# Optimization experiments

Measured on AMD Instinct MI355X. Metric: run time of the kernel, lower is better.

The kernel has to match this reference:

```python
import jax, jax.numpy as jnp
import numpy as np

D_MODEL = 1024
N_HEADS = 16
HEAD_DIM = D_MODEL // N_HEADS


def setup_inputs() -> dict:
    key = jax.random.key(0)
    k_x, k_qkv, k_out = jax.random.split(key, 3)
    B, T = 4, 2048
    x = jax.random.normal(k_x, (B, T, D_MODEL), dtype=jnp.float32)
    # nn.Linear weight is (out, in); we store transposed (in, out) for x @ W
    s = 1.0 / np.sqrt(D_MODEL)
    W_qkv = jax.random.uniform(k_qkv, (D_MODEL, 3 * D_MODEL), dtype=jnp.float32, minval=-s, maxval=s)
    W_out = jax.random.uniform(k_out, (D_MODEL, D_MODEL), dtype=jnp.float32, minval=-s, maxval=s)
    return {"x": x, "W_qkv": W_qkv, "W_out": W_out}


def reference(x, W_qkv, W_out):
    B, T, C = x.shape
    H, Dh = N_HEADS, HEAD_DIM
    qkv = x @ W_qkv                                   # (B,T,3C)
    q, k, v = jnp.split(qkv, 3, axis=-1)
    # (B,T,C) -> (B,H,T,Dh)
    def split_heads(t):
        return t.reshape(B, T, H, Dh).transpose(0, 2, 1, 3)
    q, k, v = split_heads(q), split_heads(k), split_heads(v)
    scale = 1.0 / np.sqrt(Dh).astype(np.float32)
    scores = jnp.einsum('bhqd,bhkd->bhqk', q, k) * scale  # (B,H,T,T)
    causal = jnp.triu(jnp.ones((T, T), dtype=bool), k=1)   # True above diag
    scores = jnp.where(causal, -jnp.inf, scores)
    attn = jax.nn.softmax(scores, axis=-1)
    out = jnp.einsum('bhqk,bhkd->bhqd', attn, v)       # (B,H,T,Dh)
    out = out.transpose(0, 2, 1, 3).reshape(B, T, C)
    return out @ W_out
```

## Files before the change

### kernel.cpp

```cpp
#include <hip/hip_runtime.h>
#include <stdint.h>

#define T_ 2048
#define BB_ 4

typedef __bf16 bf16x8 __attribute__((ext_vector_type(8)));
typedef float f32x4 __attribute__((ext_vector_type(4)));
typedef unsigned short u16x8 __attribute__((ext_vector_type(8)));
typedef unsigned int u32x2 __attribute__((ext_vector_type(2)));
typedef unsigned int u32x4 __attribute__((ext_vector_type(4)));

__device__ __forceinline__ unsigned short f2b(float f) {
    unsigned int u = __builtin_bit_cast(unsigned int, f);
    return (unsigned short)((u + 0x7fffu + ((u >> 16) & 1u)) >> 16);
}

__device__ __forceinline__ unsigned cvt_pk(float lo, float hi) {
    unsigned r;
    asm("v_cvt_pk_bf16_f32 %0, %1, %2" : "=v"(r) : "v"(lo), "v"(hi));
    return r;
}

__device__ __forceinline__ void gload16(const void* g, const void* lds) {
    __builtin_amdgcn_global_load_lds(
        (__attribute__((address_space(1))) void*)(uintptr_t)g,
        (__attribute__((address_space(3))) void*)(uintptr_t)(unsigned int)(uintptr_t)lds,
        16, 0, 0);
}

__device__ __forceinline__ bf16x8 ld_b8(const unsigned short* p) {
    return *(const bf16x8*)p;
}

#define MFMA16(a, b, c) __builtin_amdgcn_mfma_f32_16x16x32_bf16((a), (b), (c), 0, 0, 0)

__global__ __launch_bounds__(256) void k_cvt(const float* __restrict__ in,
                                             unsigned short* __restrict__ out, int n) {
    int i = (blockIdx.x * 256 + threadIdx.x) * 4;
    const int stride = gridDim.x * 256 * 4;
    for (; i < n; i += stride) {
        const float4 v = *(const float4*)(in + i);
        ushort4 o = make_ushort4(f2b(v.x), f2b(v.y), f2b(v.z), f2b(v.w));
        *(ushort4*)(out + i) = o;
    }
}

template <int K, int N>
__global__ __launch_bounds__(256) void k_cvt_T(const float* __restrict__ W,
                                               unsigned short* __restrict__ WT) {
    __shared__ unsigned short t_[64][72];
    const int nt = blockIdx.x % (N / 64), kt = blockIdx.x / (N / 64);
    const int tid = threadIdx.x;
    const int r = tid >> 2, c = (tid & 3) * 16;
    const float* src = W + (size_t)(kt * 64 + r) * N + nt * 64 + c;
#pragma unroll
    for (int j = 0; j < 16; j += 4) {
        float4 v = *(const float4*)(src + j);
        t_[r][c + j + 0] = f2b(v.x);
        t_[r][c + j + 1] = f2b(v.y);
        t_[r][c + j + 2] = f2b(v.z);
        t_[r][c + j + 3] = f2b(v.w);
    }
    __syncthreads();
    unsigned short* dst = WT + (size_t)(nt * 64 + r) * K + kt * 64 + c;
#pragma unroll
    for (int j = 0; j < 16; ++j) dst[j] = t_[c + j][r];
}

template <int MODE, int NCOLS>
__global__ __launch_bounds__(512, 2) void k_gemm256(
    const unsigned short* __restrict__ A, const unsigned short* __restrict__ Bt,
    void* __restrict__ Cv, unsigned short* __restrict__ vt2) {
    constexpr int K = 1024, NT = K / 64;
    __shared__ unsigned short Abuf[2][2][8192];
    __shared__ unsigned short Bbuf[2][8192];
    const int tid = threadIdx.x;
    const int lane = tid & 63, wid = tid >> 6;
    const int wr = wid >> 1, wc = wid & 1;
    const int l4 = lane >> 4, l15 = lane & 15;
    const int m0 = blockIdx.y * 256, n0 = blockIdx.x * 128;

    const int se0 = tid * 8, se1 = tid * 8 + 4096;
    const int r0_ = se0 >> 6, c0_ = (se0 & 63) ^ ((r0_ & 7) << 3);
    const int r1_ = se1 >> 6, c1_ = (se1 & 63) ^ ((r1_ & 7) << 3);

    f32x4 acc[4][4] = {};

    auto STAGE = [&](int t, int d) {
#pragma unroll
        for (int h = 0; h < 2; ++h) {
            const unsigned short* as = A + (size_t)(m0 + h * 128) * K + t * 64;
            gload16(as + (size_t)r0_ * K + c0_, &Abuf[d][h][se0]);
            gload16(as + (size_t)r1_ * K + c1_, &Abuf[d][h][se1]);
        }
        const unsigned short* bs = Bt + (size_t)n0 * K + t * 64;
        gload16(bs + (size_t)r0_ * K + c0_, &Bbuf[d][se0]);
        gload16(bs + (size_t)r1_ * K + c1_, &Bbuf[d][se1]);
    };

    auto swz = [](const unsigned short* base, int row, int col) {
        int byte = row * 128 + col * 2;
        byte ^= (row & 7) << 4;
        return (const unsigned short*)((const char*)base + byte);
    };

    STAGE(0, 0);
    STAGE(1, 1);
    for (int t = 0; t < NT; ++t) {
        if (t == NT - 1)
            asm volatile("s_waitcnt vmcnt(0)" ::: "memory");
        else
            asm volatile("s_waitcnt vmcnt(6)" ::: "memory");
        __builtin_amdgcn_sched_barrier(0);
        __builtin_amdgcn_s_barrier();
        __builtin_amdgcn_sched_barrier(0);
        const unsigned short* Ah = &Abuf[t & 1][wr >> 1][0];
        const unsigned short* Bh = &Bbuf[t & 1][0];
#pragma unroll
        for (int ks = 0; ks < 2; ++ks) {
            bf16x8 af[4], bfr[4];
#pragma unroll
            for (int m = 0; m < 4; ++m)
                af[m] = ld_b8(swz(Ah, (wr & 1) * 64 + m * 16 + l15, ks * 32 + l4 * 8));
#pragma unroll
            for (int n = 0; n < 4; ++n)
                bfr[n] = ld_b8(swz(Bh, wc * 64 + n * 16 + l15, ks * 32 + l4 * 8));
            __builtin_amdgcn_s_setprio(1);
#pragma unroll
            for (int m = 0; m < 4; ++m)
#pragma unroll
                for (int n = 0; n < 4; ++n)
                    acc[m][n] = MFMA16(af[m], bfr[n], acc[m][n]);
            __builtin_amdgcn_s_setprio(0);
            __builtin_amdgcn_sched_barrier(0);
        }
        __builtin_amdgcn_s_barrier();
        __builtin_amdgcn_sched_barrier(0);
        if (t + 2 < NT) STAGE(t + 2, t & 1);
    }

    const int crow0 = m0 + wr * 64 + l4 * 4;
    const int ccol0 = n0 + wc * 64 + l15;
    if (MODE == 0 && n0 >= 2048) {
#pragma unroll
        for (int m = 0; m < 4; ++m)
#pragma unroll
            for (int n = 0; n < 4; ++n) {
                const int row = crow0 + m * 16;
                const int c = ccol0 + n * 16 - 2048;
                const int b = row >> 11, tt = row & 2047;
                const int h = c >> 6, dh = c & 63;
                ushort4 o;
                o.x = f2b(acc[m][n][0]);
                o.y = f2b(acc[m][n][1]);
                o.z = f2b(acc[m][n][2]);
                o.w = f2b(acc[m][n][3]);
                *(ushort4*)(vt2 + (size_t)(b * 16 + h) * 131072 + (tt >> 2) * 256 +
                            dh * 4) = o;
            }
    } else {
#pragma unroll
        for (int m = 0; m < 4; ++m)
#pragma unroll
            for (int n = 0; n < 4; ++n)
#pragma unroll
                for (int r = 0; r < 4; ++r) {
                    const size_t idx =
                        (size_t)(crow0 + m * 16 + r) * NCOLS + ccol0 + n * 16;
                    if (MODE == 1)
                        ((float*)Cv)[idx] = acc[m][n][r];
                    else
                        ((unsigned short*)Cv)[idx] = f2b(acc[m][n][r]);
                }
    }
}

__global__ __launch_bounds__(256) void k_attn(const unsigned short* __restrict__ qkv,
                                              const unsigned short* __restrict__ vt2,
                                              unsigned short* __restrict__ ao) {
    __shared__ unsigned short Ks[2 * 4096];
    __shared__ unsigned short Vs[2 * 4096];
    const int bh = blockIdx.x & 63;
    const int p = blockIdx.x >> 6;
    const int b = bh >> 4, h = bh & 15;
    const int tid = threadIdx.x, lane = tid & 63, w = tid >> 6;
    const int l4 = lane >> 4, l15 = lane & 15;

    const int sr0 = w * 16 + (lane >> 3);
    const int scol = 8 * ((lane & 7) ^ (lane >> 3));
    const unsigned short* Kg = qkv + (size_t)(b * T_) * 3072 + 1024 + h * 64;

    const unsigned short* Vg = vt2 + (size_t)bh * 131072;
    const int s0v = (w * 2 + 0) * 2 + (lane >> 5);
    const int s1v = (w * 2 + 1) * 2 + (lane >> 5);
    const unsigned short* vsrc0 =
        Vg + (4 * (s0v & 3) + (s0v >> 2)) * 256 + (lane & 31) * 8;
    const unsigned short* vsrc1 =
        Vg + (4 * (s1v & 3) + (s1v >> 2)) * 256 + (lane & 31) * 8;

    for (int half = 0; half < 2; ++half) {
        const int qt = half ? p : 31 - p;

        const unsigned short* qb =
            qkv + (size_t)(b * T_ + qt * 64 + w * 16 + l15) * 3072 + h * 64;
        bf16x8 qf0, qf1;
        {
            const bf16x8 r0 = ld_b8(qb + l4 * 8);
            const bf16x8 r1 = ld_b8(qb + 32 + l4 * 8);
#pragma unroll
            for (int j = 0; j < 8; ++j) {
                qf0[j] = (__bf16)((float)r0[j] * 0.18033688f);
                qf1[j] = (__bf16)((float)r1[j] * 0.18033688f);
            }
        }

        float m_s = -1e30f, l_s = 0.f;
        f32x4 o[4] = {};

        auto STAGE = [&](int kt, int bi) {
            unsigned short* Kb = Ks + bi * 4096;
            unsigned short* Vb = Vs + bi * 4096;
            gload16(Kg + (size_t)(kt * 64 + sr0) * 3072 + scol, Kb + (w * 2) * 512);
            gload16(Kg + (size_t)(kt * 64 + sr0 + 8) * 3072 + scol, Kb + (w * 2 + 1) * 512);
            gload16(vsrc0 + kt * 4096, Vb + (w * 2) * 512);
            gload16(vsrc1 + kt * 4096, Vb + (w * 2 + 1) * 512);
        };

        auto COMPUTE = [&](int bi, bool masked) {
            const unsigned short* Kb = Ks + bi * 4096;
            const unsigned short* Vb = Vs + bi * 4096;
            float tv[4][4];
            __builtin_amdgcn_s_setprio(1);
#pragma unroll
            for (int i = 0; i < 4; ++i) {
                const int key = i * 16 + l15;
                const int sw = (key & 7) << 4;
                const bf16x8 kf0 = ld_b8(Kb + (key * 128 + ((l4 * 16) ^ sw)) / 2);
                const bf16x8 kf1 = ld_b8(Kb + (key * 128 + ((l4 * 16 + 64) ^ sw)) / 2);
                f32x4 sacc = {};
                sacc = MFMA16(kf0, qf0, sacc);
                sacc = MFMA16(kf1, qf1, sacc);
#pragma unroll
                for (int r = 0; r < 4; ++r) tv[i][r] = sacc[r];
            }
            __builtin_amdgcn_s_setprio(0);
            if (masked) {
#pragma unroll
                for (int i = 0; i < 4; ++i)
#pragma unroll
                    for (int r = 0; r < 4; ++r)
                        if (i * 16 + l4 * 4 + r > w * 16 + l15) tv[i][r] = -1e30f;
            }
            float mi[4];
#pragma unroll
            for (int i = 0; i < 4; ++i)
                mi[i] = fmaxf(fmaxf(tv[i][0], tv[i][1]), fmaxf(tv[i][2], tv[i][3]));
            float mx = fmaxf(fmaxf(mi[0], mi[1]), fmaxf(mi[2], mi[3]));
            mx = fmaxf(mx, __shfl_xor(mx, 16));
            mx = fmaxf(mx, __shfl_xor(mx, 32));
            if (__any(mx > m_s + 8.0f)) {
                const float mnew = fmaxf(m_s, mx);
                const float fac = __builtin_amdgcn_exp2f(m_s - mnew);
                m_s = mnew;
                l_s *= fac;
#pragma unroll
                for (int r = 0; r < 4; ++r) {
                    const float fr = __shfl(fac, (l4 << 4) | (l4 * 4 + r));
#pragma unroll
                    for (int ni = 0; ni < 4; ++ni) o[ni][r] *= fr;
                }
            }
            float rs = 0.f;
            unsigned pw[8];
#pragma unroll
            for (int i = 0; i < 4; ++i) {
                float pv[4];
#pragma unroll
                for (int r = 0; r < 4; ++r) {
                    pv[r] = __builtin_amdgcn_exp2f(tv[i][r] - m_s);
                    rs += pv[r];
                }
                pw[i * 2 + 0] = cvt_pk(pv[0], pv[1]);
                pw[i * 2 + 1] = cvt_pk(pv[2], pv[3]);
            }
            rs += __shfl_xor(rs, 16);
            rs += __shfl_xor(rs, 32);
            l_s += rs;
            __builtin_amdgcn_s_setprio(1);
#pragma unroll
            for (int st = 0; st < 2; ++st) {
                const u32x4 pk = {pw[st * 4 + 0], pw[st * 4 + 1], pw[st * 4 + 2],
                                  pw[st * 4 + 3]};
                const bf16x8 pf = __builtin_bit_cast(bf16x8, pk);
#pragma unroll
                for (int ni = 0; ni < 4; ++ni) {
                    const unsigned short* vb =
                        Vb + (l4 * 4 + st * 2) * 256 + (ni * 16 + l15) * 4;
                    const u32x2 va = *(const u32x2*)vb;
                    const u32x2 vc = *(const u32x2*)(vb + 256);
                    const u32x4 vv = {va.x, va.y, vc.x, vc.y};
                    const bf16x8 vf = __builtin_bit_cast(bf16x8, vv);
                    o[ni] = MFMA16(pf, vf, o[ni]);
                }
            }
            __builtin_amdgcn_s_setprio(0);
        };

        __syncthreads();
        STAGE(0, 0);
        __syncthreads();
        for (int kt = 0; kt < qt; ++kt) {
            STAGE(kt + 1, (kt + 1) & 1);
            COMPUTE(kt & 1, false);
            __syncthreads();
        }
        COMPUTE(qt & 1, true);

        unsigned short* aop = ao + (size_t)(b * T_ + qt * 64 + w * 16) * 1024 + h * 64;
#pragma unroll
        for (int r = 0; r < 4; ++r) {
            const float lr = __shfl(l_s, (l4 << 4) | (l4 * 4 + r));
            const float inv = 1.0f / lr;
#pragma unroll
            for (int ni = 0; ni < 4; ++ni)
                aop[(size_t)(l4 * 4 + r) * 1024 + ni * 16 + l15] = f2b(o[ni][r] * inv);
        }
    }
}

extern "C" void kernel_launch(void* const* d_in, const int* in_sizes, int n_in,
                              void* d_out, int out_size, void* d_ws, size_t ws_size,
                              hipStream_t stream) {
    (void)in_sizes; (void)n_in; (void)out_size; (void)ws_size;
    const float* x = (const float*)d_in[0];
    const float* Wqkv = (const float*)d_in[1];
    const float* Wout = (const float*)d_in[2];
    char* ws = (char*)d_ws;
    unsigned short* xb = (unsigned short*)(ws + 0);
    unsigned short* wqkvT = (unsigned short*)(ws + 16777216);
    unsigned short* woutT = (unsigned short*)(ws + 23068672);
    unsigned short* qkvb = (unsigned short*)(ws + 25165824);
    unsigned short* vt2 = (unsigned short*)(ws + 75497472);
    unsigned short* ao = (unsigned short*)(ws + 92274688);

    k_cvt<<<2048, 256, 0, stream>>>(x, xb, 4 * T_ * 1024);
    k_cvt_T<1024, 3072><<<16 * 48, 256, 0, stream>>>(Wqkv, wqkvT);
    k_cvt_T<1024, 1024><<<16 * 16, 256, 0, stream>>>(Wout, woutT);
    k_gemm256<0, 3072><<<dim3(24, 32), 512, 0, stream>>>(xb, wqkvT, qkvb, vt2);
    k_attn<<<1024, 256, 0, stream>>>(qkvb, vt2, ao);
    k_gemm256<1, 1024><<<dim3(8, 32), 512, 0, stream>>>(ao, woutT, d_out, nullptr);
}
```

Baseline: 168.3 us.

## Process two 64-row query tiles per attention block to reuse K/V tiles

Each attention block now handles a 128-row query tile (two 64-row sub-tiles per wave) instead of 64 rows, so every K/V tile staged into LDS feeds twice as many MFMAs. Causal masking is generalized to the two sub-tiles across the final two key tiles, and the grid is halved to 512 blocks while keeping the front/back pairing for load balance. The intent is to cut global-to-LDS traffic and per-tile sync overhead. In exchange, register pressure roughly doubles for accumulators and scores, and fewer blocks means lower parallelism on a large-CU device.

```diff
diff --git a/kernel.cpp b/kernel.cpp
--- a/kernel.cpp
+++ b/kernel.cpp
@@ -181,10 +181,11 @@
     __shared__ unsigned short Ks[2 * 4096];
     __shared__ unsigned short Vs[2 * 4096];
     const int bh = blockIdx.x & 63;
-    const int p = blockIdx.x >> 6;
+    const int p2 = blockIdx.x >> 6;
     const int b = bh >> 4, h = bh & 15;
     const int tid = threadIdx.x, lane = tid & 63, w = tid >> 6;
     const int l4 = lane >> 4, l15 = lane & 15;
+    const int wrow = w * 16 + l15;
 
     const int sr0 = w * 16 + (lane >> 3);
     const int scol = 8 * ((lane & 7) ^ (lane >> 3));
@@ -199,23 +200,24 @@
         Vg + (4 * (s1v & 3) + (s1v >> 2)) * 256 + (lane & 31) * 8;
 
     for (int half = 0; half < 2; ++half) {
-        const int qt = half ? p : 31 - p;
-
-        const unsigned short* qb =
-            qkv + (size_t)(b * T_ + qt * 64 + w * 16 + l15) * 3072 + h * 64;
-        bf16x8 qf0, qf1;
-        {
+        const int qq = half ? p2 : 15 - p2;
+
+        bf16x8 qf[2][2];
+#pragma unroll
+        for (int qa = 0; qa < 2; ++qa) {
+            const unsigned short* qb =
+                qkv + (size_t)(b * T_ + qq * 128 + qa * 64 + wrow) * 3072 + h * 64;
             const bf16x8 r0 = ld_b8(qb + l4 * 8);
             const bf16x8 r1 = ld_b8(qb + 32 + l4 * 8);
 #pragma unroll
             for (int j = 0; j < 8; ++j) {
-                qf0[j] = (__bf16)((float)r0[j] * 0.18033688f);
-                qf1[j] = (__bf16)((float)r1[j] * 0.18033688f);
-            }
-        }
-
-        float m_s = -1e30f, l_s = 0.f;
-        f32x4 o[4] = {};
+                qf[qa][0][j] = (__bf16)((float)r0[j] * 0.18033688f);
+                qf[qa][1][j] = (__bf16)((float)r1[j] * 0.18033688f);
+            }
+        }
+
+        float m_s0 = -1e30f, l_s0 = 0.f, m_s1 = -1e30f, l_s1 = 0.f;
+        f32x4 o0[4] = {}, o1[4] = {};
 
         auto STAGE = [&](int kt, int bi) {
             unsigned short* Kb = Ks + bi * 4096;
@@ -226,31 +228,7 @@
             gload16(vsrc1 + kt * 4096, Vb + (w * 2 + 1) * 512);
         };
 
-        auto COMPUTE = [&](int bi, bool masked) {
-            const unsigned short* Kb = Ks + bi * 4096;
-            const unsigned short* Vb = Vs + bi * 4096;
-            float tv[4][4];
-            __builtin_amdgcn_s_setprio(1);
-#pragma unroll
-            for (int i = 0; i < 4; ++i) {
-                const int key = i * 16 + l15;
-                const int sw = (key & 7) << 4;
-                const bf16x8 kf0 = ld_b8(Kb + (key * 128 + ((l4 * 16) ^ sw)) / 2);
-                const bf16x8 kf1 = ld_b8(Kb + (key * 128 + ((l4 * 16 + 64) ^ sw)) / 2);
-                f32x4 sacc = {};
-                sacc = MFMA16(kf0, qf0, sacc);
-                sacc = MFMA16(kf1, qf1, sacc);
-#pragma unroll
-                for (int r = 0; r < 4; ++r) tv[i][r] = sacc[r];
-            }
-            __builtin_amdgcn_s_setprio(0);
-            if (masked) {
-#pragma unroll
-                for (int i = 0; i < 4; ++i)
-#pragma unroll
-                    for (int r = 0; r < 4; ++r)
-                        if (i * 16 + l4 * 4 + r > w * 16 + l15) tv[i][r] = -1e30f;
-            }
+        auto SMAX = [&](f32x4* tv, float& m_s, float& l_s, f32x4* o, unsigned* pw) {
             float mi[4];
 #pragma unroll
             for (int i = 0; i < 4; ++i)
@@ -271,7 +249,6 @@
                 }
             }
             float rs = 0.f;
-            unsigned pw[8];
 #pragma unroll
             for (int i = 0; i < 4; ++i) {
                 float pv[4];
@@ -286,12 +263,51 @@
             rs += __shfl_xor(rs, 16);
             rs += __shfl_xor(rs, 32);
             l_s += rs;
+        };
+
+        auto COMPUTE = [&](int bi, int dk) {
+            const unsigned short* Kb = Ks + bi * 4096;
+            const unsigned short* Vb = Vs + bi * 4096;
+            f32x4 tva[4], tvb[4];
             __builtin_amdgcn_s_setprio(1);
 #pragma unroll
+            for (int i = 0; i < 4; ++i) {
+                const int key = i * 16 + l15;
+                const int sw = (key & 7) << 4;
+                const bf16x8 kf0 = ld_b8(Kb + (key * 128 + ((l4 * 16) ^ sw)) / 2);
+                const bf16x8 kf1 = ld_b8(Kb + (key * 128 + ((l4 * 16 + 64) ^ sw)) / 2);
+                f32x4 s0 = {}, s1 = {};
+                s0 = MFMA16(kf0, qf[0][0], s0);
+                s0 = MFMA16(kf1, qf[0][1], s0);
+                s1 = MFMA16(kf0, qf[1][0], s1);
+                s1 = MFMA16(kf1, qf[1][1], s1);
+                tva[i] = s0;
+                tvb[i] = s1;
+            }
+            __builtin_amdgcn_s_setprio(0);
+            if (dk >= 0) {
+                const int base = dk * 64 - wrow;
+#pragma unroll
+                for (int i = 0; i < 4; ++i)
+#pragma unroll
+                    for (int r = 0; r < 4; ++r) {
+                        const int kr = base + i * 16 + l4 * 4 + r;
+                        if (kr > 0) tva[i][r] = -1e30f;
+                        if (kr > 64) tvb[i][r] = -1e30f;
+                    }
+            }
+            unsigned pw0[8], pw1[8];
+            SMAX(tva, m_s0, l_s0, o0, pw0);
+            SMAX(tvb, m_s1, l_s1, o1, pw1);
+            __builtin_amdgcn_s_setprio(1);
+#pragma unroll
             for (int st = 0; st < 2; ++st) {
-                const u32x4 pk = {pw[st * 4 + 0], pw[st * 4 + 1], pw[st * 4 + 2],
-                                  pw[st * 4 + 3]};
-                const bf16x8 pf = __builtin_bit_cast(bf16x8, pk);
+                const u32x4 pk0 = {pw0[st * 4 + 0], pw0[st * 4 + 1], pw0[st * 4 + 2],
+                                   pw0[st * 4 + 3]};
+                const u32x4 pk1 = {pw1[st * 4 + 0], pw1[st * 4 + 1], pw1[st * 4 + 2],
+                                   pw1[st * 4 + 3]};
+                const bf16x8 pf0 = __builtin_bit_cast(bf16x8, pk0);
+                const bf16x8 pf1 = __builtin_bit_cast(bf16x8, pk1);
 #pragma unroll
                 for (int ni = 0; ni < 4; ++ni) {
                     const unsigned short* vb =
@@ -300,30 +316,40 @@
                     const u32x2 vc = *(const u32x2*)(vb + 256);
                     const u32x4 vv = {va.x, va.y, vc.x, vc.y};
                     const bf16x8 vf = __builtin_bit_cast(bf16x8, vv);
-                    o[ni] = MFMA16(pf, vf, o[ni]);
+                    o0[ni] = MFMA16(pf0, vf, o0[ni]);
+                    o1[ni] = MFMA16(pf1, vf, o1[ni]);
                 }
             }
             __builtin_amdgcn_s_setprio(0);
         };
 
+        const int NTI = 2 * qq + 1;
         __syncthreads();
         STAGE(0, 0);
         __syncthreads();
-        for (int kt = 0; kt < qt; ++kt) {
+        for (int kt = 0; kt < NTI; ++kt) {
             STAGE(kt + 1, (kt + 1) & 1);
-            COMPUTE(kt & 1, false);
+            COMPUTE(kt & 1, kt - 2 * qq);
             __syncthreads();
         }
-        COMPUTE(qt & 1, true);
-
-        unsigned short* aop = ao + (size_t)(b * T_ + qt * 64 + w * 16) * 1024 + h * 64;
-#pragma unroll
-        for (int r = 0; r < 4; ++r) {
-            const float lr = __shfl(l_s, (l4 << 4) | (l4 * 4 + r));
-            const float inv = 1.0f / lr;
-#pragma unroll
-            for (int ni = 0; ni < 4; ++ni)
-                aop[(size_t)(l4 * 4 + r) * 1024 + ni * 16 + l15] = f2b(o[ni][r] * inv);
+        COMPUTE(NTI & 1, 1);
+
+#pragma unroll
+        for (int qa = 0; qa < 2; ++qa) {
+            const float l_s = qa ? l_s1 : l_s0;
+            unsigned short* aop =
+                ao + (size_t)(b * T_ + qq * 128 + qa * 64 + w * 16) * 1024 + h * 64;
+#pragma unroll
+            for (int r = 0; r < 4; ++r) {
+                const float lr = __shfl(l_s, (l4 << 4) | (l4 * 4 + r));
+                const float inv = 1.0f / lr;
+#pragma unroll
+                for (int ni = 0; ni < 4; ++ni) {
+                    const f32x4& ov = qa ? o1[ni] : o0[ni];
+                    aop[(size_t)(l4 * 4 + r) * 1024 + ni * 16 + l15] =
+                        f2b(ov[r] * inv);
+                }
+            }
         }
     }
 }
@@ -347,6 +373,6 @@
     k_cvt_T<1024, 3072><<<16 * 48, 256, 0, stream>>>(Wqkv, wqkvT);
     k_cvt_T<1024, 1024><<<16 * 16, 256, 0, stream>>>(Wout, woutT);
     k_gemm256<0, 3072><<<dim3(24, 32), 512, 0, stream>>>(xb, wqkvT, qkvb, vt2);
-    k_attn<<<1024, 256, 0, stream>>>(qkvb, vt2, ao);
+    k_attn<<<512, 256, 0, stream>>>(qkvb, vt2, ao);
     k_gemm256<1, 1024><<<dim3(8, 32), 512, 0, stream>>>(ao, woutT, d_out, nullptr);
 }
```

Measured after the change: 170.2 us. No clear change (+1.2%).
